# Kernel optimization log

Hardware: AMD Instinct MI355X
Metric: run time of the kernel (lower is better)

## Reference

```python
import jax, jax.numpy as jnp
import numpy as np

EMBED_DIM = 512
NUM_HEADS = 64
N_WIRES = 8  # == d_k
D_K = EMBED_DIM // NUM_HEADS


def setup_inputs() -> dict:
    key = jax.random.key(0)
    k1, k2, k3, k4 = jax.random.split(key, 4)
    x = jax.random.normal(k1, (8, 2048, EMBED_DIM), dtype=jnp.float32)
    theta = jax.random.normal(k2, (N_WIRES,), dtype=jnp.float32)
    # nn.Linear(embed_dim, embed_dim): weight (out,in), bias (out,)
    W_combine = jax.random.normal(k3, (EMBED_DIM, EMBED_DIM), dtype=jnp.float32) / np.sqrt(EMBED_DIM)
    b_combine = jax.random.normal(k4, (EMBED_DIM,), dtype=jnp.float32) * 0.01
    return {"x": x, "theta": theta, "W_combine": W_combine, "b_combine": b_combine}


def reference(x, theta, W_combine, b_combine):
    b, s, e = x.shape
    h, d = NUM_HEADS, D_K
    # Quantum projection: product state, RX(x) then RX(theta) on each wire,
    # measure PauliZ  =>  <Z_i> = cos(x_i + theta_i)   (theta shared per wire)
    proj = jnp.cos(x.reshape(b, s, h, d) + theta)  # (b, s, h, d)
    # Attention as written in the source: scores over the HEAD axis per token
    scores = jnp.einsum('bshd,bsgd->bshg', proj, proj) / jnp.sqrt(jnp.float32(d))
    weights = jax.nn.softmax(scores, axis=-1)  # dropout is identity in eval
    attn = jnp.einsum('bshg,bsgd->bshd', weights, proj)  # (b, s, h, d)
    # torch: transpose(1,2).contiguous().view(b, s, e)
    attn = jnp.swapaxes(attn, 1, 2).reshape(b, s, e)
    return attn @ W_combine.T + b_combine
```

## Files before the change

### kernel.cpp

```cpp
#include <hip/hip_runtime.h>

typedef __attribute__((ext_vector_type(2))) float  f32x2;
typedef __attribute__((ext_vector_type(4))) float  f32x4;
typedef __attribute__((ext_vector_type(4))) unsigned int u32x4;
typedef _Float16 f16;
typedef __attribute__((ext_vector_type(2))) _Float16 f16x2;
typedef __attribute__((ext_vector_type(4))) _Float16 f16x4;
typedef __attribute__((ext_vector_type(8))) _Float16 f16x8;

#define S_LEN 2048
#define E_DIM 512
#define NH 64
#define DK 8

__global__ __launch_bounds__(256) void attn_stage(
    const float* __restrict__ X,
    const float* __restrict__ TH,
    const float* __restrict__ W,
    f16* __restrict__ Wb,
    f16* __restrict__ A)
{
    __shared__ __align__(16) f16 Ps[4][NH][DK];
    __shared__ __align__(16) f16 Pt[4][16][72];
    __shared__ __align__(16) f16 Ev[4][NH * NH];
    const int tid  = threadIdx.x;
    const int wv   = tid >> 6;
    const int lane = tid & 63;
    const int q    = lane >> 4;
    const int l    = lane & 15;
    const int t    = blockIdx.x * 4 + wv;

    if (blockIdx.x < 256) {
        const int i = blockIdx.x * 256 + tid;
        const float4 v = *(const float4*)(W + (size_t)i * 4);
        f16x4 o = {(f16)v.x, (f16)v.y, (f16)v.z, (f16)v.w};
        *(f16x4*)(Wb + (size_t)i * 4) = o;
    }

    const float4 t0 = *(const float4*)(TH);
    const float4 t1 = *(const float4*)(TH + 4);
    const float4 x0 = *(const float4*)(X + (size_t)t * E_DIM + lane * DK);
    const float4 x1 = *(const float4*)(X + (size_t)t * E_DIM + lane * DK + 4);

    float p[DK];
    p[0] = __cosf(x0.x + t0.x); p[1] = __cosf(x0.y + t0.y);
    p[2] = __cosf(x0.z + t0.z); p[3] = __cosf(x0.w + t0.w);
    p[4] = __cosf(x1.x + t1.x); p[5] = __cosf(x1.y + t1.y);
    p[6] = __cosf(x1.z + t1.z); p[7] = __cosf(x1.w + t1.w);

    const float cs = 0.714227053f;
    f16x8 psv;
    #pragma unroll
    for (int d = 0; d < DK; ++d) psv[d] = (f16)(p[d] * cs);
    *(f16x8*)&Ps[wv][lane][0] = psv;
    #pragma unroll
    for (int d = 0; d < DK; ++d) Pt[wv][d][lane] = (f16)p[d];
    __syncthreads();

    const f16x8 z8  = {(f16)0,(f16)0,(f16)0,(f16)0,(f16)0,(f16)0,(f16)0,(f16)0};
    const f16x8 one8= {(f16)1,(f16)1,(f16)1,(f16)1,(f16)1,(f16)1,(f16)1,(f16)1};

    f16x8 f[4];
    #pragma unroll
    for (int i = 0; i < 4; ++i) {
        const f16x8 v = *(const f16x8*)&Ps[wv][i*16 + l][0];
        f[i] = (q == 0) ? v : z8;
    }
    f32x4 St[4][4];
    #pragma unroll
    for (int i = 0; i < 4; ++i)
        #pragma unroll
        for (int jb = 0; jb < 4; ++jb) {
            f32x4 zc = {0.f, 0.f, 0.f, 0.f};
            St[i][jb] = __builtin_amdgcn_mfma_f32_16x16x32_f16(f[i], f[jb], zc, 0, 0, 0);
        }

    #pragma unroll
    for (int i = 0; i < 4; ++i)
        #pragma unroll
        for (int jb = 0; jb < 4; ++jb) {
            const float e0 = __builtin_amdgcn_exp2f(St[i][jb][0]);
            const float e1 = __builtin_amdgcn_exp2f(St[i][jb][1]);
            const float e2 = __builtin_amdgcn_exp2f(St[i][jb][2]);
            const float e3 = __builtin_amdgcn_exp2f(St[i][jb][3]);
            f16x4 w4;
            w4[0] = (f16)e0; w4[1] = (f16)e1; w4[2] = (f16)e2; w4[3] = (f16)e3;
            const int row = jb * 16 + l;
            const int c8  = (i * 2 + (q >> 1)) ^ (l & 7);
            const int col = c8 * 8 + (q & 1) * 4;
            *(f16x4*)&Ev[wv][row * 64 + col] = w4;
        }
    __syncthreads();

    f32x4 d2[4] = {};
    #pragma unroll
    for (int kh = 0; kh < 2; ++kh) {
        const f16x8 av  = *(const f16x8*)&Pt[wv][l][kh * 32 + q * 8];
        const f16x8 a2f = (l < 8) ? av : ((l == 8) ? one8 : z8);
        #pragma unroll
        for (int nb = 0; nb < 4; ++nb) {
            const int c8 = (kh * 4 + q) ^ (l & 7);
            const f16x8 bv = *(const f16x8*)&Ev[wv][(nb * 16 + l) * 64 + c8 * 8];
            d2[nb] = __builtin_amdgcn_mfma_f32_16x16x32_f16(a2f, bv, d2[nb], 0, 0, 0);
        }
    }

    float rsinv[4];
    #pragma unroll
    for (int nb = 0; nb < 4; ++nb) {
        const int rs = __builtin_amdgcn_ds_bpermute((32 + l) * 4,
                           __float_as_int(d2[nb][0]));
        rsinv[nb] = __builtin_amdgcn_rcpf(__int_as_float(rs));
    }

    if (lane < 32) {
        const int s   = t & (S_LEN - 1);
        const int cb  = (t & 63) * DK + q * 4;
        const int rb  = ((t >> 11) << 11) + (s >> 6);
        #pragma unroll
        for (int nb = 0; nb < 4; ++nb) {
            const int h   = nb * 16 + l;
            const int row = rb + h * 32;
            f16x4 o;
            #pragma unroll
            for (int r = 0; r < 4; ++r) o[r] = (f16)(d2[nb][r] * rsinv[nb]);
            *(f16x4*)(A + (size_t)row * E_DIM + cb) = o;
        }
    }
}

#define GBM 64
#define GBK 32
#define GBN 256

__global__ __launch_bounds__(256) void gemm_bias(
    const f16* __restrict__ A,
    const f16* __restrict__ W,
    const float* __restrict__ BIAS,
    float* __restrict__ OUT)
{
    __shared__ __align__(16) char ldsraw[4 * 16 * 132 * 4];
    f16*   ldsB = (f16*)ldsraw;
    f16*   ldsA = (f16*)(ldsraw + GBN * GBK * 2);
    const int tid  = threadIdx.x;
    const int lane = tid & 63;
    const int wave = tid >> 6;
    const int quad = lane >> 4;
    const int l16  = lane & 15;
    const int cg   = blockIdx.x >> 8;
    const int mg   = blockIdx.x & 255;
    const int m0   = mg * GBM;
    const int nb   = cg * GBN;
    const int wm   = wave >> 1;
    const int wnc  = (wave & 1) * 128;

    f32x4 acc[2][8] = {};

    for (int kb = 0; kb < 512; kb += GBK) {
        u32x4 wv8[4];
        int wr[4], wsx[4];
        #pragma unroll
        for (int i = 0; i < 4; ++i) {
            const int c  = tid + i * 256;
            const int r  = c >> 2;
            const int cc = c & 3;
            wr[i]  = r;
            wsx[i] = ((cc ^ (r & 3) ^ ((r >> 2) & 3))) * 8;
            wv8[i] = *(const u32x4*)(W + (size_t)(nb + r) * 512 + kb + cc * 8);
        }
        const int ar  = tid >> 2;
        const int acn = tid & 3;
        const int asx = ((acn ^ (ar & 3) ^ ((ar >> 2) & 3))) * 8;
        const u32x4 aval = *(const u32x4*)(A + (size_t)(m0 + ar) * 512 + kb + acn * 8);

        __syncthreads();
        #pragma unroll
        for (int i = 0; i < 4; ++i)
            *(u32x4*)(ldsB + wr[i] * GBK + wsx[i]) = wv8[i];
        *(u32x4*)(ldsA + ar * GBK + asx) = aval;
        __syncthreads();

        f16x8 bfr[8];
        #pragma unroll
        for (int ni = 0; ni < 8; ++ni) {
            const int rw = wnc + ni * 16 + l16;
            const int sw = ((quad ^ (rw & 3) ^ ((rw >> 2) & 3))) * 8;
            bfr[ni] = *(const f16x8*)(ldsB + rw * GBK + sw);
        }
        #pragma unroll
        for (int mi = 0; mi < 2; ++mi) {
            const int ra = wm * 32 + mi * 16 + l16;
            const int sa = ((quad ^ (ra & 3) ^ ((ra >> 2) & 3))) * 8;
            const f16x8 afr = *(const f16x8*)(ldsA + ra * GBK + sa);
            #pragma unroll
            for (int ni = 0; ni < 8; ++ni)
                acc[mi][ni] = __builtin_amdgcn_mfma_f32_16x16x32_f16(
                    afr, bfr[ni], acc[mi][ni], 0, 0, 0);
        }
    }

    float* ldsT = (float*)ldsraw + wave * (16 * 132);
    const int c4 = lane & 31;
    float4 bias4 = *(const float4*)(BIAS + nb + wnc + c4 * 4);
    #pragma unroll
    for (int mi = 0; mi < 2; ++mi) {
        __syncthreads();
        #pragma unroll
        for (int ni = 0; ni < 8; ++ni) {
            #pragma unroll
            for (int r = 0; r < 4; ++r)
                ldsT[(quad * 4 + r) * 132 + ni * 16 + l16] = acc[mi][ni][r];
        }
        __syncthreads();
        #pragma unroll
        for (int j = 0; j < 8; ++j) {
            const int row = j * 2 + (lane >> 5);
            f32x4 v = *(const f32x4*)&ldsT[row * 132 + c4 * 4];
            v.x += bias4.x; v.y += bias4.y; v.z += bias4.z; v.w += bias4.w;
            float* o = OUT + (size_t)(m0 + wm * 32 + mi * 16 + row) * 512
                           + nb + wnc + c4 * 4;
            __builtin_nontemporal_store(v, (f32x4*)o);
        }
    }
}

extern "C" void kernel_launch(void* const* d_in, const int* in_sizes, int n_in,
                              void* d_out, int out_size, void* d_ws, size_t ws_size,
                              hipStream_t stream) {
    const float* X  = (const float*)d_in[0];
    const float* TH = (const float*)d_in[1];
    const float* W  = (const float*)d_in[2];
    const float* BI = (const float*)d_in[3];
    float* OUT = (float*)d_out;

    f16* A  = (f16*)d_ws;
    f16* Wb = (f16*)((char*)d_ws + (16u << 20));

    attn_stage<<<dim3(4096), dim3(256), 0, stream>>>(X, TH, W, Wb, A);
    gemm_bias<<<dim3(512), dim3(256), 0, stream>>>(A, Wb, BI, OUT);
}
```

Measured before the change: 113.8 us.

## Stage full A row-tile in LDS once and stream W fragments from global

The GEMM now loads the block's full 64x512 A tile into swizzled LDS once with a single barrier, instead of staging A and W in LDS every 32-wide K step. Each wave owns 64 output columns and reads its W fragments directly from global memory (L2/L1) each K step, removing the per-step double barriers and LDS writes for W. This trades synchronization and LDS traffic for uncoalesced-ish direct global reads of W and 64KB LDS usage, which may lower occupancy. The epilogue is rewritten per-wave without block barriers between tiles.

Result: no change. 116.0 us (+1.9%).

```diff
diff --git a/kernel.cpp b/kernel.cpp
--- a/kernel.cpp
+++ b/kernel.cpp
@@ -130,7 +130,6 @@
 }
 
 #define GBM 64
-#define GBK 32
 #define GBN 256
 
 __global__ __launch_bounds__(256) void gemm_bias(
@@ -139,9 +138,8 @@
     const float* __restrict__ BIAS,
     float* __restrict__ OUT)
 {
-    __shared__ __align__(16) char ldsraw[4 * 16 * 132 * 4];
-    f16*   ldsB = (f16*)ldsraw;
-    f16*   ldsA = (f16*)(ldsraw + GBN * GBK * 2);
+    __shared__ __align__(16) char ldsraw[GBM * 512 * 2];
+    f16* ldsA = (f16*)ldsraw;
     const int tid  = threadIdx.x;
     const int lane = tid & 63;
     const int wave = tid >> 6;
@@ -150,75 +148,61 @@
     const int cg   = blockIdx.x >> 8;
     const int mg   = blockIdx.x & 255;
     const int m0   = mg * GBM;
-    const int nb   = cg * GBN;
-    const int wm   = wave >> 1;
-    const int wnc  = (wave & 1) * 128;
-
-    f32x4 acc[2][8] = {};
-
-    for (int kb = 0; kb < 512; kb += GBK) {
-        u32x4 wv8[4];
-        int wr[4], wsx[4];
-        #pragma unroll
-        for (int i = 0; i < 4; ++i) {
-            const int c  = tid + i * 256;
-            const int r  = c >> 2;
-            const int cc = c & 3;
-            wr[i]  = r;
-            wsx[i] = ((cc ^ (r & 3) ^ ((r >> 2) & 3))) * 8;
-            wv8[i] = *(const u32x4*)(W + (size_t)(nb + r) * 512 + kb + cc * 8);
-        }
-        const int ar  = tid >> 2;
-        const int acn = tid & 3;
-        const int asx = ((acn ^ (ar & 3) ^ ((ar >> 2) & 3))) * 8;
-        const u32x4 aval = *(const u32x4*)(A + (size_t)(m0 + ar) * 512 + kb + acn * 8);
-
-        __syncthreads();
-        #pragma unroll
-        for (int i = 0; i < 4; ++i)
-            *(u32x4*)(ldsB + wr[i] * GBK + wsx[i]) = wv8[i];
-        *(u32x4*)(ldsA + ar * GBK + asx) = aval;
-        __syncthreads();
-
-        f16x8 bfr[8];
-        #pragma unroll
-        for (int ni = 0; ni < 8; ++ni) {
-            const int rw = wnc + ni * 16 + l16;
-            const int sw = ((quad ^ (rw & 3) ^ ((rw >> 2) & 3))) * 8;
-            bfr[ni] = *(const f16x8*)(ldsB + rw * GBK + sw);
-        }
-        #pragma unroll
-        for (int mi = 0; mi < 2; ++mi) {
-            const int ra = wm * 32 + mi * 16 + l16;
-            const int sa = ((quad ^ (ra & 3) ^ ((ra >> 2) & 3))) * 8;
-            const f16x8 afr = *(const f16x8*)(ldsA + ra * GBK + sa);
+    const int colbase = cg * GBN + wave * 64;
+
+    u32x4 st[16];
+    #pragma unroll
+    for (int i = 0; i < 16; ++i) {
+        const int cid = tid + i * 256;
+        const int r = cid >> 6, c = cid & 63;
+        st[i] = *(const u32x4*)(A + (size_t)(m0 + r) * 512 + c * 8);
+    }
+    #pragma unroll
+    for (int i = 0; i < 16; ++i) {
+        const int cid = tid + i * 256;
+        const int r = cid >> 6, c = cid & 63;
+        *(u32x4*)(ldsA + r * 512 + ((c ^ (r & 7)) * 8)) = st[i];
+    }
+    __syncthreads();
+
+    f32x4 acc[4][4] = {};
+    #pragma unroll 4
+    for (int kt = 0; kt < 16; ++kt) {
+        const int kb = kt * 32;
+        f16x8 bfr[4];
+        #pragma unroll
+        for (int ni = 0; ni < 4; ++ni)
+            bfr[ni] = *(const f16x8*)(W + (size_t)(colbase + ni * 16 + l16) * 512
+                                        + kb + quad * 8);
+        #pragma unroll
+        for (int mi = 0; mi < 4; ++mi) {
+            const int ra = mi * 16 + l16;
+            const int cc = ((kb >> 3) + quad) ^ (ra & 7);
+            const f16x8 afr = *(const f16x8*)(ldsA + ra * 512 + cc * 8);
             #pragma unroll
-            for (int ni = 0; ni < 8; ++ni)
+            for (int ni = 0; ni < 4; ++ni)
                 acc[mi][ni] = __builtin_amdgcn_mfma_f32_16x16x32_f16(
                     afr, bfr[ni], acc[mi][ni], 0, 0, 0);
         }
     }
-
-    float* ldsT = (float*)ldsraw + wave * (16 * 132);
-    const int c4 = lane & 31;
-    float4 bias4 = *(const float4*)(BIAS + nb + wnc + c4 * 4);
-    #pragma unroll
-    for (int mi = 0; mi < 2; ++mi) {
-        __syncthreads();
-        #pragma unroll
-        for (int ni = 0; ni < 8; ++ni) {
+    __syncthreads();
+
+    float* ldsT = (float*)ldsraw + wave * (16 * 68);
+    float4 bias4 = *(const float4*)(BIAS + colbase + l16 * 4);
+    #pragma unroll
+    for (int mi = 0; mi < 4; ++mi) {
+        #pragma unroll
+        for (int ni = 0; ni < 4; ++ni)
             #pragma unroll
             for (int r = 0; r < 4; ++r)
-                ldsT[(quad * 4 + r) * 132 + ni * 16 + l16] = acc[mi][ni][r];
-        }
-        __syncthreads();
-        #pragma unroll
-        for (int j = 0; j < 8; ++j) {
-            const int row = j * 2 + (lane >> 5);
-            f32x4 v = *(const f32x4*)&ldsT[row * 132 + c4 * 4];
+                ldsT[(quad * 4 + r) * 68 + ni * 16 + l16] = acc[mi][ni][r];
+        #pragma unroll
+        for (int j = 0; j < 4; ++j) {
+            const int row = j * 4 + quad;
+            f32x4 v = *(const f32x4*)&ldsT[row * 68 + l16 * 4];
             v.x += bias4.x; v.y += bias4.y; v.z += bias4.z; v.w += bias4.w;
-            float* o = OUT + (size_t)(m0 + wm * 32 + mi * 16 + row) * 512
-                           + nb + wnc + c4 * 4;
+            float* o = OUT + (size_t)(m0 + mi * 16 + row) * 512
+                           + colbase + l16 * 4;
             __builtin_nontemporal_store(v, (f32x4*)o);
         }
     }
```
